# Performance work log

Hardware: AMD Instinct MI355X
Metric: run time of the kernel (lower is better)

## Reference

```python
import jax, jax.numpy as jnp
import numpy as np

N = 50000      # nodes
E = 800000     # edges
IN = 128       # raw node feature dim
EMB = 64       # gene/pathway embedding dim
H = 256        # hidden dim
R = 12         # relations
B = 8          # num_bases (hardcoded in HRAN)
HEADS = 4      # attention heads (hardcoded)
NG = 20000     # n_gene
NPATH = 2000   # n_path
IN1 = IN + EMB # conv1 input dim


def _glorot(k, shape):
    fan_in, fan_out = shape[-2], shape[-1]
    s = np.sqrt(2.0 / (fan_in + fan_out)).astype(np.float32)
    return jax.random.normal(k, shape, jnp.float32) * s


def setup_inputs() -> dict:
    key = jax.random.key(0)
    ks = jax.random.split(key, 20)
    return {
        "x": jax.random.normal(ks[0], (N, IN), jnp.float32),
        "edge_index": jax.random.randint(ks[1], (2, E), 0, N),
        "edge_type": jax.random.randint(ks[2], (E,), 0, R),
        "gene_idx": jnp.arange(NG),
        "path_idx": jnp.arange(NPATH) + NG,  # disjoint from gene_idx
        "gene_emb": jax.random.normal(ks[3], (NG, EMB), jnp.float32) * 0.02,
        "path_emb": jax.random.normal(ks[4], (NPATH, EMB), jnp.float32) * 0.02,
        "comp1": _glorot(ks[5], (R, B)),
        "basis1": _glorot(ks[6], (B, IN1, H)),
        "root1": _glorot(ks[7], (IN1, H)),
        "bias1": jnp.zeros((H,), jnp.float32),
        "att1": _glorot(ks[8], (HEADS, H // HEADS)),
        "comp2": _glorot(ks[9], (R, B)),
        "basis2": _glorot(ks[10], (B, H, H)),
        "root2": _glorot(ks[11], (H, H)),
        "bias2": jnp.zeros((H,), jnp.float32),
        "att2": _glorot(ks[12], (HEADS, H // HEADS)),
        "pred_w": _glorot(ks[13], (H, 12)),
        "pred_b": jnp.zeros((12,), jnp.float32),
    }


def _rgcn(x, src, dst, et, comp, basis, root, bias):
    # Basis-decomposed RGCN with per-relation mean aggregation (PyG default).
    flat = dst * R + et                                   # combined (node, rel) id
    cnt = jax.ops.segment_sum(jnp.ones((src.shape[0],), jnp.float32), flat,
                              num_segments=N * R)
    w = 1.0 / jnp.maximum(cnt[flat], 1.0)                 # [E] mean normalizer
    coeff = comp[et] * w[:, None]                         # [E, B]
    xs = x[src]                                           # [E, in]  gather
    # aggregate in input space, then one dense contraction with the bases
    agg = jnp.stack([jax.ops.segment_sum(coeff[:, b, None] * xs, dst,
                                         num_segments=N)
                     for b in range(B)], axis=1)          # [N, B, in]
    return jnp.einsum('nbi,bio->no', agg, basis) + x @ root + bias


def _hran_conv(x, src, dst, et, comp, basis, root, bias, att):
    h = _rgcn(x, src, dst, et, comp, basis, root, bias)
    h = h.reshape(N, HEADS, -1)                           # [N, heads, hd]
    alpha = jax.nn.softmax((h * att).sum(-1), axis=1)     # softmax over heads
    return (h * alpha[..., None]).reshape(N, -1)


def reference(x, edge_index, edge_type, gene_idx, path_idx,
              gene_emb, path_emb,
              comp1, basis1, root1, bias1, att1,
              comp2, basis2, root2, bias2, att2,
              pred_w, pred_b):
    src, dst = edge_index[0], edge_index[1]
    x0 = jnp.concatenate([x, jnp.zeros((N, EMB), x.dtype)], axis=1)
    x0 = x0.at[gene_idx, IN:].add(gene_emb)
    x0 = x0.at[path_idx, IN:].add(path_emb)
    h = _hran_conv(x0, src, dst, edge_type, comp1, basis1, root1, bias1, att1)
    h = _hran_conv(h, src, dst, edge_type, comp2, basis2, root2, bias2, att2)
    return h @ pred_w + pred_b                            # [N, 12]
```

## Files before the change

### kernel.cpp

```cpp
#include <hip/hip_runtime.h>
#include <cstddef>

#define NN     50000
#define NE     800000
#define IND    128
#define EMBD   64
#define IN1    192
#define HDIM   256
#define RR     12
#define BB     8
#define NGENE  20000
#define NPATH  2000
#define NRK    (RR * NN)
#define SCB    1024
#define NSB    ((NRK + SCB - 1) / SCB)
#define CH0    25088

typedef __attribute__((ext_vector_type(8))) short short8;
typedef __attribute__((ext_vector_type(4))) float f32x4;
typedef unsigned short ushortT;
typedef __attribute__((address_space(3))) void lds_void;
typedef __attribute__((address_space(1))) const void glb_void;

__device__ __forceinline__ float bu2f(unsigned short u) {
  unsigned int x = ((unsigned int)u) << 16;
  return __builtin_bit_cast(float, x);
}
__device__ __forceinline__ unsigned short f2bu(float f) {
  unsigned int x = __builtin_bit_cast(unsigned int, f);
  unsigned int r = (x + 0x7fffu + ((x >> 16) & 1u)) >> 16;
  return (unsigned short)r;
}


__global__ void k_build_x0(const float* __restrict__ x, ushortT* __restrict__ x0) {
  int t = blockIdx.x * 256 + threadIdx.x;
  if (t >= NN * IN1) return;
  int n = t / IN1, i = t - n * IN1;
  float v = (i < IND) ? x[(size_t)n * IND + i] : 0.0f;
  int kt = i >> 6, ch = (i >> 3) & 7, off = i & 7;
  x0[(size_t)n * IN1 + kt * 64 + ((ch ^ (n & 7)) * 8) + off] = f2bu(v);
}

__global__ void k_add_emb(const int* __restrict__ idx, const float* __restrict__ emb,
                          ushortT* __restrict__ x0, int count) {
  int t = blockIdx.x * 256 + threadIdx.x;
  if (t >= count * EMBD) return;
  int g = t / EMBD, j = t - g * EMBD;
  int n = idx[g];
  int ch = (j >> 3) & 7, off = j & 7;
  x0[(size_t)n * IN1 + 128 + ((ch ^ (n & 7)) * 8) + off] = f2bu(emb[t]);
}

__global__ void k_count(const int* __restrict__ ei, const int* __restrict__ et,
                        int* __restrict__ cnt) {
  int e = blockIdx.x * 256 + threadIdx.x;
  if (e >= NE) return;
  atomicAdd(&cnt[ei[NE + e] * RR + et[e]], 1);
}

__global__ __launch_bounds__(256) void k_scan1(const int* __restrict__ cnt,
                                               int* __restrict__ bsum) {
  __shared__ int lds[256];
  int t = threadIdx.x;
  int base = blockIdx.x * SCB + t * 4;
  int s = 0;
#pragma unroll
  for (int j = 0; j < 4; j++) { int idx = base + j; if (idx < NRK) s += cnt[idx]; }
  lds[t] = s; __syncthreads();
  for (int d = 128; d > 0; d >>= 1) { if (t < d) lds[t] += lds[t + d]; __syncthreads(); }
  if (t == 0) bsum[blockIdx.x] = lds[0];
}

__global__ __launch_bounds__(1024) void k_scan2(const int* __restrict__ bsum,
                                                int* __restrict__ bscan) {
  __shared__ int lds[1024];
  int t = threadIdx.x;
  int v = (t < NSB) ? bsum[t] : 0;
  lds[t] = v; __syncthreads();
  for (int d = 1; d < 1024; d <<= 1) {
    int add = (t >= d) ? lds[t - d] : 0; __syncthreads();
    lds[t] += add; __syncthreads();
  }
  if (t < NSB) bscan[t] = lds[t] - v;
}

__global__ __launch_bounds__(256) void k_scan3(const int* __restrict__ cnt,
                                               const int* __restrict__ bscan,
                                               int* __restrict__ off) {
  __shared__ int lds[256];
  int t = threadIdx.x;
  int base = blockIdx.x * SCB + t * 4;
  int v[4]; int s = 0;
#pragma unroll
  for (int j = 0; j < 4; j++) { int idx = base + j; v[j] = (idx < NRK) ? cnt[idx] : 0; s += v[j]; }
  lds[t] = s; __syncthreads();
  for (int d = 1; d < 256; d <<= 1) {
    int add = (t >= d) ? lds[t - d] : 0; __syncthreads();
    lds[t] += add; __syncthreads();
  }
  int ex = lds[t] - s + bscan[blockIdx.x];
#pragma unroll
  for (int j = 0; j < 4; j++) {
    int idx = base + j;
    if (idx < NRK) { off[idx] = ex; ex += v[j]; }
  }
}

__global__ void k_fill(const int* __restrict__ ei, const int* __restrict__ et,
                       const int* __restrict__ off, int* __restrict__ fill,
                       int* __restrict__ srcs) {
  int e = blockIdx.x * 256 + threadIdx.x;
  if (e >= NE) return;
  int key = ei[NE + e] * RR + et[e];
  int pos = off[key] + atomicAdd(&fill[key], 1);
  srcs[pos] = ei[e];
}

__global__ void k_wbasis(const float* __restrict__ basis, ushortT* __restrict__ W,
                         int in_dim) {
  int t = blockIdx.x * 256 + threadIdx.x;
  int total = BB * HDIM * in_dim;
  if (t >= total) return;
  int i = t % in_dim;
  int o = (t / in_dim) & 255;
  int b = t / (in_dim * 256);
  W[t] = f2bu(basis[((size_t)b * in_dim + i) * HDIM + o]);
}

__global__ void k_troot(const float* __restrict__ root, ushortT* __restrict__ rt,
                        int in_dim) {
  int t = blockIdx.x * 256 + threadIdx.x;
  if (t >= in_dim * HDIM) return;
  int i = t % in_dim, o = t / in_dim;
  rt[t] = f2bu(root[(size_t)i * HDIM + o]);
}

__global__ __launch_bounds__(256) void k_aggb(const int* __restrict__ srcs,
                                              const int* __restrict__ off,
                                              const int* __restrict__ cnt,
                                              const float* __restrict__ comp,
                                              const ushortT* __restrict__ xin,
                                              ushortT* __restrict__ aggB,
                                              int in_dim, int row0, int nrows) {
  int wv = threadIdx.x >> 6;
  int lane = threadIdx.x & 63;
  int li = blockIdx.x * 4 + wv;
  if (li >= nrows) return;
  int dst = row0 + li;
  bool act = lane * 4 < in_dim;
  int kt = lane >> 4, chl = (lane >> 1) & 7, offh = (lane & 1) * 4;
  int kbase = kt * 64 + offh;

  int beg[RR], n[RR];
#pragma unroll
  for (int rl = 0; rl < RR; rl++) {
    beg[rl] = off[dst * RR + rl];
    n[rl]   = cnt[dst * RR + rl];
  }

  float acc[BB][4];
#pragma unroll
  for (int b = 0; b < BB; b++)
#pragma unroll
    for (int e = 0; e < 4; e++) acc[b][e] = 0.f;

  for (int rl = 0; rl < RR; rl++) {
    int ne = n[rl];
    if (ne == 0) continue;
    int bg = beg[rl];
    float s0 = 0.f, s1 = 0.f, s2 = 0.f, s3 = 0.f;
    int p = 0;
    for (; p + 2 <= ne; p += 2) {
      int sa = srcs[bg + p];
      int sb = srcs[bg + p + 1];
      if (act) {
        ushort4 va = *(const ushort4*)(xin + (size_t)sa * in_dim + kbase + ((chl ^ (sa & 7)) * 8));
        ushort4 vb = *(const ushort4*)(xin + (size_t)sb * in_dim + kbase + ((chl ^ (sb & 7)) * 8));
        s0 += bu2f(va.x); s1 += bu2f(va.y); s2 += bu2f(va.z); s3 += bu2f(va.w);
        s0 += bu2f(vb.x); s1 += bu2f(vb.y); s2 += bu2f(vb.z); s3 += bu2f(vb.w);
      }
    }
    if (p < ne) {
      int sa = srcs[bg + p];
      if (act) {
        ushort4 va = *(const ushort4*)(xin + (size_t)sa * in_dim + kbase + ((chl ^ (sa & 7)) * 8));
        s0 += bu2f(va.x); s1 += bu2f(va.y); s2 += bu2f(va.z); s3 += bu2f(va.w);
      }
    }
    float wn = 1.0f / (float)ne;
#pragma unroll
    for (int b = 0; b < BB; b++) {
      float cb = comp[rl * BB + b] * wn;
      acc[b][0] += cb * s0; acc[b][1] += cb * s1;
      acc[b][2] += cb * s2; acc[b][3] += cb * s3;
    }
  }

  if (act) {
    size_t base = (size_t)li * BB * in_dim;
    int swz = (chl ^ (dst & 7)) * 8;
#pragma unroll
    for (int b = 0; b < BB; b++) {
      ushort4 o;
      o.x = f2bu(acc[b][0]); o.y = f2bu(acc[b][1]);
      o.z = f2bu(acc[b][2]); o.w = f2bu(acc[b][3]);
      *(ushort4*)(aggB + base + (size_t)b * in_dim + kbase + swz) = o;
    }
  }
}

__global__ __launch_bounds__(256, 2) void k_gemm(const ushortT* __restrict__ xin,
                                                 const ushortT* __restrict__ aggB,
                                                 const ushortT* __restrict__ W,
                                                 const float* __restrict__ bias,
                                                 const float* __restrict__ att,
                                                 ushortT* __restrict__ hout,
                                                 int in_dim, int row0, int row1) {
  __shared__ ushortT As[4][64 * 64];
  __shared__ float sm[64][4];
  const int tid = threadIdx.x;
  const int bm = row0 + blockIdx.x * 64;
  const int wv = tid >> 6, l = tid & 63;
  const int wc = wv;
  const int lm = l & 15, lq = l >> 4;
  const int nkt = in_dim >> 6;
  const int totKt = 9 * nkt;

  f32x4 acc[4][4];
#pragma unroll
  for (int mt = 0; mt < 4; mt++)
#pragma unroll
    for (int nt = 0; nt < 4; nt++) acc[mt][nt] = (f32x4){0.f, 0.f, 0.f, 0.f};

  auto stage = [&](int buf, int seg, int kt) {
#pragma unroll
    for (int j = 0; j < 2; j++) {
      int r = wv * 16 + j * 8;
      int g = bm + r + (l >> 3); if (g >= row1) g = row1 - 1;
      const ushortT* gp;
      if (seg == 0) gp = xin + (size_t)g * in_dim + kt * 64 + (l & 7) * 8;
      else gp = aggB + ((size_t)(g - row0) * 8 + (seg - 1)) * in_dim + kt * 64 + (l & 7) * 8;
      ushortT* lp = &As[buf][r * 64];
      __builtin_amdgcn_global_load_lds((glb_void*)gp, (lds_void*)lp, 16, 0, 0);
    }
  };

  auto mfmaTile = [&](int buf, int segC, int ktC) {
    short8 bf[2][4];
    const ushortT* wt = W + (size_t)(wc * 64 + lm) * in_dim +
                        (size_t)segC * 256 * in_dim + ktC * 64 + lq * 8;
#pragma unroll
    for (int nt = 0; nt < 4; nt++) {
      bf[0][nt] = *(const short8*)(wt + (size_t)nt * 16 * in_dim);
      bf[1][nt] = *(const short8*)(wt + (size_t)nt * 16 * in_dim + 32);
    }
#pragma unroll
    for (int ks = 0; ks < 2; ks++) {
      short8 af[4];
#pragma unroll
      for (int mt = 0; mt < 4; mt++) {
        int ar = mt * 16 + lm;
        af[mt] = *(const short8*)(&As[buf][ar * 64 + (((ks * 4) + lq) ^ (ar & 7)) * 8]);
      }
#pragma unroll
      for (int mt = 0; mt < 4; mt++)
#pragma unroll
        for (int nt = 0; nt < 4; nt++)
          acc[mt][nt] = __builtin_amdgcn_mfma_f32_16x16x32_bf16(af[mt], bf[ks][nt],
                                                                acc[mt][nt], 0, 0, 0);
    }
  };

  int segL = 0, ktL = 0, segP = 0, ktP = 0;
  auto bump = [&](int& s, int& k) { if (++k == nkt) { k = 0; s++; } };

  stage(0, segP, ktP); bump(segP, ktP);
  stage(1, segP, ktP); bump(segP, ktP);
  stage(2, segP, ktP);
  int sidx = 2;

  for (int t = 0; t < totKt; t++) {
    asm volatile("s_waitcnt vmcnt(4)" ::: "memory");
    __builtin_amdgcn_s_barrier();
    __builtin_amdgcn_sched_barrier(0);
    if (sidx < totKt - 1) { bump(segP, ktP); sidx++; }
    stage((t + 3) & 3, segP, ktP);
    mfmaTile(t & 3, segL, ktL);
    bump(segL, ktL);
  }
  asm volatile("s_waitcnt vmcnt(0)" ::: "memory");
  __syncthreads();

  float bv[4];
#pragma unroll
  for (int nt = 0; nt < 4; nt++) bv[nt] = bias[wc * 64 + nt * 16 + lm];
#pragma unroll
  for (int mt = 0; mt < 4; mt++)
#pragma unroll
    for (int nt = 0; nt < 4; nt++)
#pragma unroll
      for (int r = 0; r < 4; r++) acc[mt][nt][r] += bv[nt];

  float av[4];
#pragma unroll
  for (int nt = 0; nt < 4; nt++) av[nt] = att[wc * 64 + nt * 16 + lm];
#pragma unroll
  for (int mt = 0; mt < 4; mt++) {
    float sr[4];
#pragma unroll
    for (int r = 0; r < 4; r++)
      sr[r] = acc[mt][0][r] * av[0] + acc[mt][1][r] * av[1] +
              acc[mt][2][r] * av[2] + acc[mt][3][r] * av[3];
#pragma unroll
    for (int o = 1; o <= 8; o <<= 1) {
#pragma unroll
      for (int r = 0; r < 4; r++) sr[r] += __shfl_xor(sr[r], o, 64);
    }
    if (lm == 0) {
#pragma unroll
      for (int r = 0; r < 4; r++) sm[mt * 16 + lq * 4 + r][wc] = sr[r];
    }
  }
  __syncthreads();
  if (tid < 64) {
    float s0 = sm[tid][0], s1 = sm[tid][1], s2 = sm[tid][2], s3 = sm[tid][3];
    float mx = fmaxf(fmaxf(s0, s1), fmaxf(s2, s3));
    float e0 = __expf(s0 - mx), e1 = __expf(s1 - mx), e2 = __expf(s2 - mx), e3 = __expf(s3 - mx);
    float inv = 1.0f / (e0 + e1 + e2 + e3);
    sm[tid][0] = e0 * inv; sm[tid][1] = e1 * inv; sm[tid][2] = e2 * inv; sm[tid][3] = e3 * inv;
  }
  __syncthreads();
#pragma unroll
  for (int mt = 0; mt < 4; mt++) {
#pragma unroll
    for (int r = 0; r < 4; r++) {
      int rl = mt * 16 + lq * 4 + r;
      int row = bm + rl;
      if (row >= row1) continue;
      float al = sm[rl][wc];
      ushortT* op = hout + (size_t)row * HDIM + wc * 64;
      int key = row & 7;
#pragma unroll
      for (int nt = 0; nt < 4; nt++) {
        int ci = nt * 16 + lm;
        op[(((ci >> 3) ^ key) * 8) + (ci & 7)] = f2bu(acc[mt][nt][r] * al);
      }
    }
  }
}

__global__ void k_pred(const ushortT* __restrict__ h, const float* __restrict__ w,
                       const float* __restrict__ b, float* __restrict__ out) {
  int t = blockIdx.x * 256 + threadIdx.x;
  if (t >= NN * 12) return;
  int n = t / 12, j = t - n * 12;
  float acc = b[j];
  const ushortT* hp = h + (size_t)n * HDIM;
  int key = n & 7;
#pragma unroll
  for (int kt = 0; kt < 4; kt++)
#pragma unroll
    for (int cs = 0; cs < 8; cs++) {
      int ch = cs ^ key;
      int kb = kt * 64 + ch * 8;
      const ushortT* hh = hp + kt * 64 + cs * 8;
#pragma unroll
      for (int o = 0; o < 8; o++) acc += bu2f(hh[o]) * w[(kb + o) * 12 + j];
    }
  out[t] = acc;
}

extern "C" void kernel_launch(void* const* d_in, const int* in_sizes, int n_in,
                              void* d_out, int out_size, void* d_ws, size_t ws_size,
                              hipStream_t stream) {
  const float* x         = (const float*)d_in[0];
  const int*   edge_idx  = (const int*)d_in[1];
  const int*   edge_type = (const int*)d_in[2];
  const int*   gene_idx  = (const int*)d_in[3];
  const int*   path_idx  = (const int*)d_in[4];
  const float* gene_emb  = (const float*)d_in[5];
  const float* path_emb  = (const float*)d_in[6];
  const float* comp1     = (const float*)d_in[7];
  const float* basis1    = (const float*)d_in[8];
  const float* root1     = (const float*)d_in[9];
  const float* bias1     = (const float*)d_in[10];
  const float* att1      = (const float*)d_in[11];
  const float* comp2     = (const float*)d_in[12];
  const float* basis2    = (const float*)d_in[13];
  const float* root2     = (const float*)d_in[14];
  const float* bias2     = (const float*)d_in[15];
  const float* att2      = (const float*)d_in[16];
  const float* pred_w    = (const float*)d_in[17];
  const float* pred_b    = (const float*)d_in[18];
  float* out = (float*)d_out;

  char* ws = (char*)d_ws;
  ushortT* x0b   = (ushortT*)(ws);
  ushortT* h2b   = (ushortT*)(ws);
  ushortT* h1b   = (ushortT*)(ws + 25600000);
  ushortT* aggB  = (ushortT*)(ws + 51200000);
  ushortT* Wb1   = (ushortT*)(ws + 154000000);
  ushortT* Wb2   = (ushortT*)(ws + 155000000);
  int*     cnt   = (int*)(ws + 156200000);
  int*     off   = (int*)(ws + 158600000);
  int*     srcs  = (int*)(ws + 161000000);
  int*     fill  = (int*)(ws + 164200000);
  int*     bsum  = (int*)(ws + 166600000);
  int*     bscan = (int*)(ws + 166608000);

  dim3 blk(256);

  k_build_x0<<<dim3((NN * IN1) / 256), blk, 0, stream>>>(x, x0b);
  k_add_emb<<<dim3((NGENE * EMBD) / 256), blk, 0, stream>>>(gene_idx, gene_emb, x0b, NGENE);
  k_add_emb<<<dim3((NPATH * EMBD) / 256), blk, 0, stream>>>(path_idx, path_emb, x0b, NPATH);
  hipMemsetAsync(cnt, 0, NRK * 4, stream);
  hipMemsetAsync(fill, 0, NRK * 4, stream);
  k_count<<<dim3(NE / 256), blk, 0, stream>>>(edge_idx, edge_type, cnt);
  k_scan1<<<dim3(NSB), blk, 0, stream>>>(cnt, bsum);
  k_scan2<<<dim3(1), dim3(1024), 0, stream>>>(bsum, bscan);
  k_scan3<<<dim3(NSB), blk, 0, stream>>>(cnt, bscan, off);
  k_fill<<<dim3(NE / 256), blk, 0, stream>>>(edge_idx, edge_type, off, fill, srcs);
  k_troot<<<dim3((IN1 * HDIM) / 256), blk, 0, stream>>>(root1, Wb1, IN1);
  k_troot<<<dim3((HDIM * HDIM) / 256), blk, 0, stream>>>(root2, Wb2, HDIM);
  k_wbasis<<<dim3((BB * HDIM * IN1) / 256), blk, 0, stream>>>(basis1, Wb1 + 256 * IN1, IN1);
  k_wbasis<<<dim3((BB * HDIM * HDIM) / 256), blk, 0, stream>>>(basis2, Wb2 + 256 * HDIM, HDIM);

  const int r1 = CH0, n1 = CH0;
  const int n2 = NN - CH0;
  const int g1 = n1 / 64;
  const int g2 = (n2 + 63) / 64;

  k_aggb<<<dim3(n1 / 4), blk, 0, stream>>>(srcs, off, cnt, comp1, x0b, aggB, IN1, 0, n1);
  k_gemm<<<dim3(g1), blk, 0, stream>>>(x0b, aggB, Wb1, bias1, att1, h1b, IN1, 0, r1);
  k_aggb<<<dim3(n2 / 4), blk, 0, stream>>>(srcs, off, cnt, comp1, x0b, aggB, IN1, r1, n2);
  k_gemm<<<dim3(g2), blk, 0, stream>>>(x0b, aggB, Wb1, bias1, att1, h1b, IN1, r1, NN);

  k_aggb<<<dim3(n1 / 4), blk, 0, stream>>>(srcs, off, cnt, comp2, h1b, aggB, HDIM, 0, n1);
  k_gemm<<<dim3(g1), blk, 0, stream>>>(h1b, aggB, Wb2, bias2, att2, h2b, HDIM, 0, r1);
  k_aggb<<<dim3(n2 / 4), blk, 0, stream>>>(srcs, off, cnt, comp2, h1b, aggB, HDIM, r1, n2);
  k_gemm<<<dim3(g2), blk, 0, stream>>>(h1b, aggB, Wb2, bias2, att2, h2b, HDIM, r1, NN);

  k_pred<<<dim3((NN * 12 + 255) / 256), blk, 0, stream>>>(h2b, pred_w, pred_b, out);
}
```

Measured before the change: 821.6 us.

## Flatten per-node edge loop with precomputed edge coefficients; double-buffer GEMM weight fragments

The aggregation kernel now walks all of a node's incoming edges in one flat loop, four edges at a time with source indices prefetched. Each edge carries a precomputed 8-wide basis coefficient (comp times the mean normaliser), built by a new per-layer kernel from relation and weight arrays written during CSR fill. This removes the per-relation loop with its many short, divergent iterations, at the cost of 8x more FMAs per edge and an extra 25.6MB coefficient array read per layer. The GEMM now loads the next K-tile's weight fragments into a second register set before the barrier, overlapping B-operand global loads with the MFMAs. That raises register pressure and adjusts the vmcnt wait.

```diff
diff --git a/kernel.cpp b/kernel.cpp
--- a/kernel.cpp
+++ b/kernel.cpp
@@ -108,13 +108,25 @@
 }
 
 __global__ void k_fill(const int* __restrict__ ei, const int* __restrict__ et,
-                       const int* __restrict__ off, int* __restrict__ fill,
-                       int* __restrict__ srcs) {
+                       const int* __restrict__ off, const int* __restrict__ cnt,
+                       int* __restrict__ fill, int* __restrict__ srcs,
+                       int* __restrict__ erel, float* __restrict__ ewgt) {
   int e = blockIdx.x * 256 + threadIdx.x;
   if (e >= NE) return;
-  int key = ei[NE + e] * RR + et[e];
+  int r = et[e];
+  int key = ei[NE + e] * RR + r;
   int pos = off[key] + atomicAdd(&fill[key], 1);
   srcs[pos] = ei[e];
+  erel[pos] = r;
+  ewgt[pos] = 1.0f / (float)cnt[key];
+}
+
+__global__ void k_ecoef(const int* __restrict__ erel, const float* __restrict__ ewgt,
+                        const float* __restrict__ comp, float* __restrict__ ecoef) {
+  int t = blockIdx.x * 256 + threadIdx.x;
+  if (t >= NE * 8) return;
+  int e = t >> 3, b = t & 7;
+  ecoef[t] = comp[erel[e] * BB + b] * ewgt[e];
 }
 
 __global__ void k_wbasis(const float* __restrict__ basis, ushortT* __restrict__ W,
@@ -138,8 +150,7 @@
 
 __global__ __launch_bounds__(256) void k_aggb(const int* __restrict__ srcs,
                                               const int* __restrict__ off,
-                                              const int* __restrict__ cnt,
-                                              const float* __restrict__ comp,
+                                              const float* __restrict__ ecoef,
                                               const ushortT* __restrict__ xin,
                                               ushortT* __restrict__ aggB,
                                               int in_dim, int row0, int nrows) {
@@ -152,12 +163,9 @@
   int kt = lane >> 4, chl = (lane >> 1) & 7, offh = (lane & 1) * 4;
   int kbase = kt * 64 + offh;
 
-  int beg[RR], n[RR];
-#pragma unroll
-  for (int rl = 0; rl < RR; rl++) {
-    beg[rl] = off[dst * RR + rl];
-    n[rl]   = cnt[dst * RR + rl];
-  }
+  int e0 = off[dst * RR];
+  int e1 = (dst + 1 < NN) ? off[(dst + 1) * RR] : NE;
+  int tot = e1 - e0;
 
   float acc[BB][4];
 #pragma unroll
@@ -165,35 +173,47 @@
 #pragma unroll
     for (int e = 0; e < 4; e++) acc[b][e] = 0.f;
 
-  for (int rl = 0; rl < RR; rl++) {
-    int ne = n[rl];
-    if (ne == 0) continue;
-    int bg = beg[rl];
-    float s0 = 0.f, s1 = 0.f, s2 = 0.f, s3 = 0.f;
-    int p = 0;
-    for (; p + 2 <= ne; p += 2) {
-      int sa = srcs[bg + p];
-      int sb = srcs[bg + p + 1];
-      if (act) {
-        ushort4 va = *(const ushort4*)(xin + (size_t)sa * in_dim + kbase + ((chl ^ (sa & 7)) * 8));
-        ushort4 vb = *(const ushort4*)(xin + (size_t)sb * in_dim + kbase + ((chl ^ (sb & 7)) * 8));
-        s0 += bu2f(va.x); s1 += bu2f(va.y); s2 += bu2f(va.z); s3 += bu2f(va.w);
-        s0 += bu2f(vb.x); s1 += bu2f(vb.y); s2 += bu2f(vb.z); s3 += bu2f(vb.w);
-      }
-    }
-    if (p < ne) {
-      int sa = srcs[bg + p];
-      if (act) {
-        ushort4 va = *(const ushort4*)(xin + (size_t)sa * in_dim + kbase + ((chl ^ (sa & 7)) * 8));
-        s0 += bu2f(va.x); s1 += bu2f(va.y); s2 += bu2f(va.z); s3 += bu2f(va.w);
-      }
-    }
-    float wn = 1.0f / (float)ne;
-#pragma unroll
-    for (int b = 0; b < BB; b++) {
-      float cb = comp[rl * BB + b] * wn;
-      acc[b][0] += cb * s0; acc[b][1] += cb * s1;
-      acc[b][2] += cb * s2; acc[b][3] += cb * s3;
+  auto gaddr = [&](int s) {
+    return xin + (size_t)s * in_dim + kbase + ((chl ^ (s & 7)) * 8);
+  };
+  auto fma8 = [&](const ushort4& v, const float4& ca, const float4& cb) {
+    float xv[4] = {bu2f(v.x), bu2f(v.y), bu2f(v.z), bu2f(v.w)};
+    float cc[8] = {ca.x, ca.y, ca.z, ca.w, cb.x, cb.y, cb.z, cb.w};
+#pragma unroll
+    for (int b = 0; b < 8; b++)
+#pragma unroll
+      for (int e = 0; e < 4; e++) acc[b][e] += cc[b] * xv[e];
+  };
+
+  int s0 = (0 < tot) ? srcs[e0 + 0] : 0;
+  int s1 = (1 < tot) ? srcs[e0 + 1] : 0;
+  int s2 = (2 < tot) ? srcs[e0 + 2] : 0;
+  int s3 = (3 < tot) ? srcs[e0 + 3] : 0;
+
+  for (int p = 0; p < tot; p += 4) {
+    int m = tot - p;
+    ushort4 v0{}, v1{}, v2{}, v3{};
+    if (act) {
+      v0 = *(const ushort4*)gaddr(s0);
+      if (m > 1) v1 = *(const ushort4*)gaddr(s1);
+      if (m > 2) v2 = *(const ushort4*)gaddr(s2);
+      if (m > 3) v3 = *(const ushort4*)gaddr(s3);
+    }
+    const float* cp = ecoef + (size_t)(e0 + p) * 8;
+    float4 a0 = *(const float4*)(cp), b0 = *(const float4*)(cp + 4);
+    float4 a1{}, b1{}, a2{}, b2{}, a3{}, b3{};
+    if (m > 1) { a1 = *(const float4*)(cp + 8);  b1 = *(const float4*)(cp + 12); }
+    if (m > 2) { a2 = *(const float4*)(cp + 16); b2 = *(const float4*)(cp + 20); }
+    if (m > 3) { a3 = *(const float4*)(cp + 24); b3 = *(const float4*)(cp + 28); }
+    s0 = (p + 4 < tot) ? srcs[e0 + p + 4] : 0;
+    s1 = (p + 5 < tot) ? srcs[e0 + p + 5] : 0;
+    s2 = (p + 6 < tot) ? srcs[e0 + p + 6] : 0;
+    s3 = (p + 7 < tot) ? srcs[e0 + p + 7] : 0;
+    if (act) {
+      fma8(v0, a0, b0);
+      if (m > 1) fma8(v1, a1, b1);
+      if (m > 2) fma8(v2, a2, b2);
+      if (m > 3) fma8(v3, a3, b3);
     }
   }
 
@@ -233,6 +253,9 @@
 #pragma unroll
     for (int nt = 0; nt < 4; nt++) acc[mt][nt] = (f32x4){0.f, 0.f, 0.f, 0.f};
 
+  struct WF { short8 f[2][4]; };
+  WF w0, w1;
+
   auto stage = [&](int buf, int seg, int kt) {
 #pragma unroll
     for (int j = 0; j < 2; j++) {
@@ -246,15 +269,17 @@
     }
   };
 
-  auto mfmaTile = [&](int buf, int segC, int ktC) {
-    short8 bf[2][4];
+  auto loadW = [&](WF& wd, int seg, int kt) {
     const ushortT* wt = W + (size_t)(wc * 64 + lm) * in_dim +
-                        (size_t)segC * 256 * in_dim + ktC * 64 + lq * 8;
+                        (size_t)seg * 256 * in_dim + kt * 64 + lq * 8;
 #pragma unroll
     for (int nt = 0; nt < 4; nt++) {
-      bf[0][nt] = *(const short8*)(wt + (size_t)nt * 16 * in_dim);
-      bf[1][nt] = *(const short8*)(wt + (size_t)nt * 16 * in_dim + 32);
-    }
+      wd.f[0][nt] = *(const short8*)(wt + (size_t)nt * 16 * in_dim);
+      wd.f[1][nt] = *(const short8*)(wt + (size_t)nt * 16 * in_dim + 32);
+    }
+  };
+
+  auto mfmaT = [&](int buf, const WF& wf) {
 #pragma unroll
     for (int ks = 0; ks < 2; ks++) {
       short8 af[4];
@@ -267,28 +292,37 @@
       for (int mt = 0; mt < 4; mt++)
 #pragma unroll
         for (int nt = 0; nt < 4; nt++)
-          acc[mt][nt] = __builtin_amdgcn_mfma_f32_16x16x32_bf16(af[mt], bf[ks][nt],
+          acc[mt][nt] = __builtin_amdgcn_mfma_f32_16x16x32_bf16(af[mt], wf.f[ks][nt],
                                                                 acc[mt][nt], 0, 0, 0);
     }
   };
 
-  int segL = 0, ktL = 0, segP = 0, ktP = 0;
-  auto bump = [&](int& s, int& k) { if (++k == nkt) { k = 0; s++; } };
-
-  stage(0, segP, ktP); bump(segP, ktP);
-  stage(1, segP, ktP); bump(segP, ktP);
-  stage(2, segP, ktP);
-  int sidx = 2;
-
-  for (int t = 0; t < totKt; t++) {
-    asm volatile("s_waitcnt vmcnt(4)" ::: "memory");
+  int segS = 0, ktS = 0;
+  int segW = 0, ktW = 0;
+  auto bumpC = [&](int& s, int& k) {
+    if (++k == nkt) { k = 0; if (++s == 9) { s = 8; k = nkt - 1; } }
+  };
+
+  auto body = [&](int t, WF& wuse, WF& wload) {
+    loadW(wload, segW, ktW); bumpC(segW, ktW);
+    asm volatile("s_waitcnt vmcnt(10)" ::: "memory");
     __builtin_amdgcn_s_barrier();
     __builtin_amdgcn_sched_barrier(0);
-    if (sidx < totKt - 1) { bump(segP, ktP); sidx++; }
-    stage((t + 3) & 3, segP, ktP);
-    mfmaTile(t & 3, segL, ktL);
-    bump(segL, ktL);
-  }
+    stage((t + 3) & 3, segS, ktS); bumpC(segS, ktS);
+    mfmaT(t & 3, wuse);
+  };
+
+  stage(0, segS, ktS); bumpC(segS, ktS);
+  stage(1, segS, ktS); bumpC(segS, ktS);
+  stage(2, segS, ktS); bumpC(segS, ktS);
+  loadW(w0, segW, ktW); bumpC(segW, ktW);
+
+  int t = 0;
+  for (; t + 1 < totKt; t += 2) {
+    body(t, w0, w1);
+    body(t + 1, w1, w0);
+  }
+  if (t < totKt) body(t, w0, w1);
   asm volatile("s_waitcnt vmcnt(0)" ::: "memory");
   __syncthreads();
 
@@ -408,6 +442,9 @@
   int*     fill  = (int*)(ws + 164200000);
   int*     bsum  = (int*)(ws + 166600000);
   int*     bscan = (int*)(ws + 166608000);
+  int*     erel  = (int*)(ws + 166616000);
+  float*   ewgt  = (float*)(ws + 169816000);
+  float*   ecoef = (float*)(ws + 173016000);
 
   dim3 blk(256);
 
@@ -420,7 +457,7 @@
   k_scan1<<<dim3(NSB), blk, 0, stream>>>(cnt, bsum);
   k_scan2<<<dim3(1), dim3(1024), 0, stream>>>(bsum, bscan);
   k_scan3<<<dim3(NSB), blk, 0, stream>>>(cnt, bscan, off);
-  k_fill<<<dim3(NE / 256), blk, 0, stream>>>(edge_idx, edge_type, off, fill, srcs);
+  k_fill<<<dim3(NE / 256), blk, 0, stream>>>(edge_idx, edge_type, off, cnt, fill, srcs, erel, ewgt);
   k_troot<<<dim3((IN1 * HDIM) / 256), blk, 0, stream>>>(root1, Wb1, IN1);
   k_troot<<<dim3((HDIM * HDIM) / 256), blk, 0, stream>>>(root2, Wb2, HDIM);
   k_wbasis<<<dim3((BB * HDIM * IN1) / 256), blk, 0, stream>>>(basis1, Wb1 + 256 * IN1, IN1);
@@ -431,14 +468,16 @@
   const int g1 = n1 / 64;
   const int g2 = (n2 + 63) / 64;
 
-  k_aggb<<<dim3(n1 / 4), blk, 0, stream>>>(srcs, off, cnt, comp1, x0b, aggB, IN1, 0, n1);
+  k_ecoef<<<dim3(NE * 8 / 256), blk, 0, stream>>>(erel, ewgt, comp1, ecoef);
+  k_aggb<<<dim3(n1 / 4), blk, 0, stream>>>(srcs, off, ecoef, x0b, aggB, IN1, 0, n1);
   k_gemm<<<dim3(g1), blk, 0, stream>>>(x0b, aggB, Wb1, bias1, att1, h1b, IN1, 0, r1);
-  k_aggb<<<dim3(n2 / 4), blk, 0, stream>>>(srcs, off, cnt, comp1, x0b, aggB, IN1, r1, n2);
+  k_aggb<<<dim3(n2 / 4), blk, 0, stream>>>(srcs, off, ecoef, x0b, aggB, IN1, r1, n2);
   k_gemm<<<dim3(g2), blk, 0, stream>>>(x0b, aggB, Wb1, bias1, att1, h1b, IN1, r1, NN);
 
-  k_aggb<<<dim3(n1 / 4), blk, 0, stream>>>(srcs, off, cnt, comp2, h1b, aggB, HDIM, 0, n1);
+  k_ecoef<<<dim3(NE * 8 / 256), blk, 0, stream>>>(erel, ewgt, comp2, ecoef);
+  k_aggb<<<dim3(n1 / 4), blk, 0, stream>>>(srcs, off, ecoef, h1b, aggB, HDIM, 0, n1);
   k_gemm<<<dim3(g1), blk, 0, stream>>>(h1b, aggB, Wb2, bias2, att2, h2b, HDIM, 0, r1);
-  k_aggb<<<dim3(n2 / 4), blk, 0, stream>>>(srcs, off, cnt, comp2, h1b, aggB, HDIM, r1, n2);
+  k_aggb<<<dim3(n2 / 4), blk, 0, stream>>>(srcs, off, ecoef, h1b, aggB, HDIM, r1, n2);
   k_gemm<<<dim3(g2), blk, 0, stream>>>(h1b, aggB, Wb2, bias2, att2, h2b, HDIM, r1, NN);
 
   k_pred<<<dim3((NN * 12 + 255) / 256), blk, 0, stream>>>(h2b, pred_w, pred_b, out);
```

After: 892.8 us. 8.7% more time.

## Load GEMM A operands directly from global into registers, dropping the LDS staging

Applied to the files above, without the earlier changes.

The GEMM kernel no longer stages A tiles into shared memory with async global-to-LDS loads and barriers. Each wave now loads its A and W fragments straight from global memory into registers, using a three-deep register rotation to overlap loads with MFMA. This removes LDS traffic and block-wide barriers, but each of the four waves now fetches the same A rows redundantly, and register pressure goes up. The loop relies on the step count being a multiple of three, and it clamps the final bump.

```diff
diff --git a/kernel.cpp b/kernel.cpp
--- a/kernel.cpp
+++ b/kernel.cpp
@@ -19,8 +19,6 @@
 typedef __attribute__((ext_vector_type(8))) short short8;
 typedef __attribute__((ext_vector_type(4))) float f32x4;
 typedef unsigned short ushortT;
-typedef __attribute__((address_space(3))) void lds_void;
-typedef __attribute__((address_space(1))) const void glb_void;
 
 __device__ __forceinline__ float bu2f(unsigned short u) {
   unsigned int x = ((unsigned int)u) << 16;
@@ -217,7 +215,6 @@
                                                  const float* __restrict__ att,
                                                  ushortT* __restrict__ hout,
                                                  int in_dim, int row0, int row1) {
-  __shared__ ushortT As[4][64 * 64];
   __shared__ float sm[64][4];
   const int tid = threadIdx.x;
   const int bm = row0 + blockIdx.x * 64;
@@ -225,7 +222,7 @@
   const int wc = wv;
   const int lm = l & 15, lq = l >> 4;
   const int nkt = in_dim >> 6;
-  const int totKt = 9 * nkt;
+  const int totS = 18 * nkt;
 
   f32x4 acc[4][4];
 #pragma unroll
@@ -233,64 +230,66 @@
 #pragma unroll
     for (int nt = 0; nt < 4; nt++) acc[mt][nt] = (f32x4){0.f, 0.f, 0.f, 0.f};
 
-  auto stage = [&](int buf, int seg, int kt) {
-#pragma unroll
-    for (int j = 0; j < 2; j++) {
-      int r = wv * 16 + j * 8;
-      int g = bm + r + (l >> 3); if (g >= row1) g = row1 - 1;
-      const ushortT* gp;
-      if (seg == 0) gp = xin + (size_t)g * in_dim + kt * 64 + (l & 7) * 8;
-      else gp = aggB + ((size_t)(g - row0) * 8 + (seg - 1)) * in_dim + kt * 64 + (l & 7) * 8;
-      ushortT* lp = &As[buf][r * 64];
-      __builtin_amdgcn_global_load_lds((glb_void*)gp, (lds_void*)lp, 16, 0, 0);
+  int ar[4]; const ushortT* abase[4]; int c0u[4];
+#pragma unroll
+  for (int mt = 0; mt < 4; mt++) {
+    int g = bm + mt * 16 + lm; if (g >= row1) g = row1 - 1;
+    ar[mt] = g;
+    abase[mt] = xin + (size_t)g * in_dim;
+    c0u[mt] = (lq ^ (g & 7)) * 8;
+  }
+
+  int segC = 0, ktC = 0, ksC = 0;
+  auto bump = [&]() {
+    if (++ksC == 2) {
+      ksC = 0;
+      if (++ktC == nkt) {
+        ktC = 0; ++segC;
+        if (segC == 9) { segC = 8; ktC = nkt - 1; ksC = 1; }
+        else if (segC == 1) {
+#pragma unroll
+          for (int mt = 0; mt < 4; mt++)
+            abase[mt] = aggB + (size_t)(ar[mt] - row0) * 8 * in_dim;
+        } else {
+#pragma unroll
+          for (int mt = 0; mt < 4; mt++) abase[mt] += in_dim;
+        }
+      }
     }
   };
 
-  auto mfmaTile = [&](int buf, int segC, int ktC) {
-    short8 bf[2][4];
-    const ushortT* wt = W + (size_t)(wc * 64 + lm) * in_dim +
-                        (size_t)segC * 256 * in_dim + ktC * 64 + lq * 8;
-#pragma unroll
-    for (int nt = 0; nt < 4; nt++) {
-      bf[0][nt] = *(const short8*)(wt + (size_t)nt * 16 * in_dim);
-      bf[1][nt] = *(const short8*)(wt + (size_t)nt * 16 * in_dim + 32);
-    }
-#pragma unroll
-    for (int ks = 0; ks < 2; ks++) {
-      short8 af[4];
-#pragma unroll
-      for (int mt = 0; mt < 4; mt++) {
-        int ar = mt * 16 + lm;
-        af[mt] = *(const short8*)(&As[buf][ar * 64 + (((ks * 4) + lq) ^ (ar & 7)) * 8]);
-      }
-#pragma unroll
-      for (int mt = 0; mt < 4; mt++)
-#pragma unroll
-        for (int nt = 0; nt < 4; nt++)
-          acc[mt][nt] = __builtin_amdgcn_mfma_f32_16x16x32_bf16(af[mt], bf[ks][nt],
-                                                                acc[mt][nt], 0, 0, 0);
-    }
+  auto ldA = [&](short8* d) {
+    int ko = ktC * 64, xs = ksC * 32;
+#pragma unroll
+    for (int mt = 0; mt < 4; mt++)
+      d[mt] = *(const short8*)(abase[mt] + ko + (c0u[mt] ^ xs));
   };
-
-  int segL = 0, ktL = 0, segP = 0, ktP = 0;
-  auto bump = [&](int& s, int& k) { if (++k == nkt) { k = 0; s++; } };
-
-  stage(0, segP, ktP); bump(segP, ktP);
-  stage(1, segP, ktP); bump(segP, ktP);
-  stage(2, segP, ktP);
-  int sidx = 2;
-
-  for (int t = 0; t < totKt; t++) {
-    asm volatile("s_waitcnt vmcnt(4)" ::: "memory");
-    __builtin_amdgcn_s_barrier();
-    __builtin_amdgcn_sched_barrier(0);
-    if (sidx < totKt - 1) { bump(segP, ktP); sidx++; }
-    stage((t + 3) & 3, segP, ktP);
-    mfmaTile(t & 3, segL, ktL);
-    bump(segL, ktL);
-  }
-  asm volatile("s_waitcnt vmcnt(0)" ::: "memory");
-  __syncthreads();
+  auto ldW = [&](short8* d) {
+    const ushortT* p = W + ((size_t)segC * 256 + wc * 64 + lm) * in_dim +
+                       ktC * 64 + ksC * 32 + lq * 8;
+#pragma unroll
+    for (int nt = 0; nt < 4; nt++) d[nt] = *(const short8*)(p + (size_t)nt * 16 * in_dim);
+  };
+  auto doM = [&](short8* a, short8* w) {
+#pragma unroll
+    for (int mt = 0; mt < 4; mt++)
+#pragma unroll
+      for (int nt = 0; nt < 4; nt++)
+        acc[mt][nt] = __builtin_amdgcn_mfma_f32_16x16x32_bf16(a[mt], w[nt],
+                                                              acc[mt][nt], 0, 0, 0);
+  };
+
+  short8 a0[4], w0f[4], a1[4], w1f[4], a2[4], w2f[4];
+  ldA(a0); ldW(w0f); bump();
+  ldA(a1); ldW(w1f); bump();
+  for (int t = 0; t < totS; t += 3) {
+    ldA(a2); ldW(w2f); bump();
+    doM(a0, w0f);
+    ldA(a0); ldW(w0f); bump();
+    doM(a1, w1f);
+    ldA(a1); ldW(w1f); bump();
+    doM(a2, w2f);
+  }
 
   float bv[4];
 #pragma unroll
```

Result: slower. 842.3 us (+2.5%).

## Prefetch first two neighbor rows per relation and double-buffer weight fragments

Applied to the files above, without the earlier changes.

In the aggregation kernel, the first two source indices and feature rows for all 12 relations are loaded up front. This exposes more independent memory requests before the accumulation loop starts. In the GEMM kernel, the weight (B) fragments are now loaded one k-tile ahead into alternating register sets, and the vmcnt wait is adjusted to match. This overlaps global weight loads with MFMA work. The cost is higher register pressure (24 ushort4 prefetch slots plus two weight fragment sets), which may reduce occupancy.

```diff
diff --git a/kernel.cpp b/kernel.cpp
--- a/kernel.cpp
+++ b/kernel.cpp
@@ -152,6 +152,10 @@
   int kt = lane >> 4, chl = (lane >> 1) & 7, offh = (lane & 1) * 4;
   int kbase = kt * 64 + offh;
 
+  auto gaddr = [&](int s) {
+    return (const ushort4*)(xin + (size_t)s * in_dim + kbase + ((chl ^ (s & 7)) * 8));
+  };
+
   int beg[RR], n[RR];
 #pragma unroll
   for (int rl = 0; rl < RR; rl++) {
@@ -159,33 +163,44 @@
     n[rl]   = cnt[dst * RR + rl];
   }
 
+  int sa[RR], sb[RR];
+#pragma unroll
+  for (int rl = 0; rl < RR; rl++) {
+    sa[rl] = (n[rl] > 0) ? srcs[beg[rl]] : 0;
+    sb[rl] = (n[rl] > 1) ? srcs[beg[rl] + 1] : 0;
+  }
+
+  ushort4 va[RR], vb[RR];
+  if (act) {
+#pragma unroll
+    for (int rl = 0; rl < RR; rl++) va[rl] = *gaddr(sa[rl]);
+#pragma unroll
+    for (int rl = 0; rl < RR; rl++) vb[rl] = *gaddr(sb[rl]);
+  }
+
   float acc[BB][4];
 #pragma unroll
   for (int b = 0; b < BB; b++)
 #pragma unroll
     for (int e = 0; e < 4; e++) acc[b][e] = 0.f;
 
+#pragma unroll
   for (int rl = 0; rl < RR; rl++) {
     int ne = n[rl];
     if (ne == 0) continue;
-    int bg = beg[rl];
     float s0 = 0.f, s1 = 0.f, s2 = 0.f, s3 = 0.f;
-    int p = 0;
-    for (; p + 2 <= ne; p += 2) {
-      int sa = srcs[bg + p];
-      int sb = srcs[bg + p + 1];
+    if (act) {
+      s0 = bu2f(va[rl].x); s1 = bu2f(va[rl].y); s2 = bu2f(va[rl].z); s3 = bu2f(va[rl].w);
+      if (ne > 1) {
+        s0 += bu2f(vb[rl].x); s1 += bu2f(vb[rl].y);
+        s2 += bu2f(vb[rl].z); s3 += bu2f(vb[rl].w);
+      }
+    }
+    for (int p = 2; p < ne; p++) {
+      int s = srcs[beg[rl] + p];
       if (act) {
-        ushort4 va = *(const ushort4*)(xin + (size_t)sa * in_dim + kbase + ((chl ^ (sa & 7)) * 8));
-        ushort4 vb = *(const ushort4*)(xin + (size_t)sb * in_dim + kbase + ((chl ^ (sb & 7)) * 8));
-        s0 += bu2f(va.x); s1 += bu2f(va.y); s2 += bu2f(va.z); s3 += bu2f(va.w);
-        s0 += bu2f(vb.x); s1 += bu2f(vb.y); s2 += bu2f(vb.z); s3 += bu2f(vb.w);
-      }
-    }
-    if (p < ne) {
-      int sa = srcs[bg + p];
-      if (act) {
-        ushort4 va = *(const ushort4*)(xin + (size_t)sa * in_dim + kbase + ((chl ^ (sa & 7)) * 8));
-        s0 += bu2f(va.x); s1 += bu2f(va.y); s2 += bu2f(va.z); s3 += bu2f(va.w);
+        ushort4 v = *gaddr(s);
+        s0 += bu2f(v.x); s1 += bu2f(v.y); s2 += bu2f(v.z); s3 += bu2f(v.w);
       }
     }
     float wn = 1.0f / (float)ne;
@@ -233,6 +248,9 @@
 #pragma unroll
     for (int nt = 0; nt < 4; nt++) acc[mt][nt] = (f32x4){0.f, 0.f, 0.f, 0.f};
 
+  struct WF { short8 f[2][4]; };
+  WF w0, w1;
+
   auto stage = [&](int buf, int seg, int kt) {
 #pragma unroll
     for (int j = 0; j < 2; j++) {
@@ -246,15 +264,17 @@
     }
   };
 
-  auto mfmaTile = [&](int buf, int segC, int ktC) {
-    short8 bf[2][4];
+  auto loadW = [&](WF& wd, int seg, int kt) {
     const ushortT* wt = W + (size_t)(wc * 64 + lm) * in_dim +
-                        (size_t)segC * 256 * in_dim + ktC * 64 + lq * 8;
+                        (size_t)seg * 256 * in_dim + kt * 64 + lq * 8;
 #pragma unroll
     for (int nt = 0; nt < 4; nt++) {
-      bf[0][nt] = *(const short8*)(wt + (size_t)nt * 16 * in_dim);
-      bf[1][nt] = *(const short8*)(wt + (size_t)nt * 16 * in_dim + 32);
-    }
+      wd.f[0][nt] = *(const short8*)(wt + (size_t)nt * 16 * in_dim);
+      wd.f[1][nt] = *(const short8*)(wt + (size_t)nt * 16 * in_dim + 32);
+    }
+  };
+
+  auto mfmaT = [&](int buf, const WF& wf) {
 #pragma unroll
     for (int ks = 0; ks < 2; ks++) {
       short8 af[4];
@@ -267,28 +287,37 @@
       for (int mt = 0; mt < 4; mt++)
 #pragma unroll
         for (int nt = 0; nt < 4; nt++)
-          acc[mt][nt] = __builtin_amdgcn_mfma_f32_16x16x32_bf16(af[mt], bf[ks][nt],
+          acc[mt][nt] = __builtin_amdgcn_mfma_f32_16x16x32_bf16(af[mt], wf.f[ks][nt],
                                                                 acc[mt][nt], 0, 0, 0);
     }
   };
 
-  int segL = 0, ktL = 0, segP = 0, ktP = 0;
-  auto bump = [&](int& s, int& k) { if (++k == nkt) { k = 0; s++; } };
-
-  stage(0, segP, ktP); bump(segP, ktP);
-  stage(1, segP, ktP); bump(segP, ktP);
-  stage(2, segP, ktP);
-  int sidx = 2;
-
-  for (int t = 0; t < totKt; t++) {
-    asm volatile("s_waitcnt vmcnt(4)" ::: "memory");
+  int segS = 0, ktS = 0;
+  int segW = 0, ktW = 0;
+  auto bumpC = [&](int& s, int& k) {
+    if (++k == nkt) { k = 0; if (++s == 9) { s = 8; k = nkt - 1; } }
+  };
+
+  auto body = [&](int t, WF& wuse, WF& wload) {
+    loadW(wload, segW, ktW); bumpC(segW, ktW);
+    asm volatile("s_waitcnt vmcnt(10)" ::: "memory");
     __builtin_amdgcn_s_barrier();
     __builtin_amdgcn_sched_barrier(0);
-    if (sidx < totKt - 1) { bump(segP, ktP); sidx++; }
-    stage((t + 3) & 3, segP, ktP);
-    mfmaTile(t & 3, segL, ktL);
-    bump(segL, ktL);
-  }
+    stage((t + 3) & 3, segS, ktS); bumpC(segS, ktS);
+    mfmaT(t & 3, wuse);
+  };
+
+  stage(0, segS, ktS); bumpC(segS, ktS);
+  stage(1, segS, ktS); bumpC(segS, ktS);
+  stage(2, segS, ktS); bumpC(segS, ktS);
+  loadW(w0, segW, ktW); bumpC(segW, ktW);
+
+  int t = 0;
+  for (; t + 1 < totKt; t += 2) {
+    body(t, w0, w1);
+    body(t + 1, w1, w0);
+  }
+  if (t < totKt) body(t, w0, w1);
   asm volatile("s_waitcnt vmcnt(0)" ::: "memory");
   __syncthreads();
 
```

Measured after the change: 791.0 us. 3.7% less time.
